# Optimization experiments

Measured on AMD Instinct MI355X. Metric: run time of the kernel, lower is better.

The kernel has to match this reference:

```python
import jax, jax.numpy as jnp
import numpy as np

_CLAMP = 1e6  # clamp bound for real/imag parts after each eml level
CPLX = jnp.complex64


def _eml_op(u, v):
    # eml(u, v) = exp(log(u) * log(v)) in complex arithmetic
    return jnp.exp(jnp.log(u) * jnp.log(v))


def _sanitize(z):
    r = jnp.clip(jnp.nan_to_num(z.real, nan=0.0, posinf=_CLAMP, neginf=-_CLAMP), -_CLAMP, _CLAMP)
    i = jnp.clip(jnp.nan_to_num(z.imag, nan=0.0, posinf=_CLAMP, neginf=-_CLAMP), -_CLAMP, _CLAMP)
    return jax.lax.complex(r, i)


def setup_inputs() -> dict:
    key = jax.random.key(0)
    k1, k2, k3 = jax.random.split(key, 3)
    depth = 10
    n_leaves = 2 ** depth          # 1024
    n_internal = n_leaves - 1      # 1023
    init_scale = 0.1
    batch = 65536
    x = jax.random.normal(k1, (batch,), jnp.float32)
    leaf = jax.random.normal(k2, (n_leaves, 2), jnp.float32) * init_scale
    leaf = leaf.at[:, 0].add(1.0)  # leaf_init[:, 0] += 1.0
    gate = jax.random.normal(k3, (n_internal, 2, 3), jnp.float32) * init_scale
    gate = gate.at[..., 2].add(1.0)  # gate_init[..., 2] += 1.0
    return {"x": x, "leaf_logits": leaf, "gate_logits": gate}


def reference(x, leaf_logits, gate_logits):
    xc = x.astype(CPLX)                      # [B]
    a = leaf_logits[:, 0].astype(CPLX)       # [L]
    b = leaf_logits[:, 1].astype(CPLX)       # [L]
    level = a[None, :] + b[None, :] * xc[:, None]   # [B, L] leaf inputs: alpha + beta*x
    x_b = xc[:, None]                        # [B, 1]
    g_all = gate_logits.astype(CPLX)         # [L-1, 2, 3]
    node_idx = 0
    while level.shape[1] > 1:
        n_pairs = level.shape[1] // 2
        left = level[:, 0::2]                # [B, n_pairs]
        right = level[:, 1::2]
        g = g_all[node_idx:node_idx + n_pairs]
        left_in = g[:, 0, 0][None] + g[:, 0, 1][None] * x_b + g[:, 0, 2][None] * left
        right_in = g[:, 1, 0][None] + g[:, 1, 1][None] * x_b + g[:, 1, 2][None] * right
        level = _sanitize(_eml_op(left_in, right_in))
        node_idx += n_pairs
    return level[:, 0]                       # [B] complex64
```

## Files before the change

kernel.cpp:

```cpp
#include <hip/hip_runtime.h>
#include <math.h>

#define CLAMPV 1000000.0f
#define PI_F     3.14159274f
#define HALFPI_F 1.57079633f
#define LN2_F    0.69314718f
#define L2E_F    1.44269504f
#define C1_F     0.17328680f
#define C2_F     0.05515890f
#define C2R_F    0.11031780f

typedef float v2f __attribute__((ext_vector_type(2)));

__device__ __forceinline__ v2f vb(float s) { return (v2f){s, s}; }
__device__ __forceinline__ v2f vfma(v2f a, v2f b, v2f c) { return __builtin_elementwise_fma(a, b, c); }

__device__ __forceinline__ const float* gptr(const float* __restrict__ g, int node) {
    return g + 6 * __builtin_amdgcn_readfirstlane(node);
}

__device__ __forceinline__ unsigned sortkey(float x) {
    unsigned u = __float_as_uint(x);
    u ^= (unsigned)(((int)u) >> 31) | 0x80000000u;
    return u;
}

__device__ __forceinline__ unsigned rank_below(unsigned long long m) {
    return __builtin_amdgcn_mbcnt_hi((unsigned)(m >> 32),
           __builtin_amdgcn_mbcnt_lo((unsigned)m, 0u));
}

__device__ __forceinline__ v2f fnode(v2f l, v2f r, v2f x,
                                     const float* __restrict__ g, v2f& tmin) {
    float g0 = g[0], g1 = g[1], g2 = g[2], g3 = g[3], g4 = g[4], g5 = g[5];
    v2f u = vfma(vb(g2), l, vfma(vb(g1), x, vb(g0)));
    v2f v = vfma(vb(g5), r, vfma(vb(g4), x, vb(g3)));
    tmin = __builtin_elementwise_min(tmin, __builtin_elementwise_min(u, v));
    v2f L2u = (v2f){__builtin_amdgcn_logf(u.x), __builtin_amdgcn_logf(u.y)};
    v2f L2v = (v2f){__builtin_amdgcn_logf(v.x), __builtin_amdgcn_logf(v.y)};
    v2f e = (vb(LN2_F) * L2u) * L2v;
    v2f rr = (v2f){__builtin_amdgcn_exp2f(e.x), __builtin_amdgcn_exp2f(e.y)};
    return __builtin_elementwise_min(rr, vb(CLAMPV));
}

__global__ __launch_bounds__(1024, 8) void eml_fast_taint(
    const float* __restrict__ x_g, const float* __restrict__ leaf_g,
    const float* __restrict__ gate_g, float* __restrict__ out,
    unsigned* __restrict__ cnt, unsigned* __restrict__ list,
    int batch, int out_real_only)
{
    __shared__ float4 s_t[16][64];

    const int lane = threadIdx.x;
    const int s    = threadIdx.y;
    const int e0 = blockIdx.x * 128 + lane;
    const v2f x2 = (v2f){x_g[e0], x_g[e0 + 64]};

    v2f tmin = vb(1.0f);
    v2f cA, cB, root;

#pragma clang loop unroll(disable)
    for (int q = 0; q < 4; ++q) {
        const int jq = 64 * s + 16 * q;
        v2f r2[2], h1, c;
#pragma unroll
        for (int p = 0; p < 4; ++p) {
            const int j = jq + 4 * p;
            const float* L = leaf_g + 2 * __builtin_amdgcn_readfirstlane(j);
            v2f l0 = vfma(vb(L[1]), x2, vb(L[0]));
            v2f l1 = vfma(vb(L[3]), x2, vb(L[2]));
            v2f l2 = vfma(vb(L[5]), x2, vb(L[4]));
            v2f l3 = vfma(vb(L[7]), x2, vb(L[6]));

            v2f A  = fnode(l0, l1, x2, gptr(gate_g, j >> 1), tmin);
            v2f B  = fnode(l2, l3, x2, gptr(gate_g, (j >> 1) + 1), tmin);
            v2f r1 = fnode(A, B, x2, gptr(gate_g, 512 + (j >> 2)), tmin);
            if (p & 1) r2[p >> 1] = fnode(h1, r1, x2, gptr(gate_g, 768 + (j >> 3)), tmin);
            else       h1 = r1;
        }
        c = fnode(r2[0], r2[1], x2, gptr(gate_g, 896 + (jq >> 4)), tmin);
        if      (q == 0) cA = c;
        else if (q == 1) cB = fnode(cA, c, x2, gptr(gate_g, 960 + 2 * s), tmin);
        else if (q == 2) cA = c;
        else {
            v2f t = fnode(cA, c, x2, gptr(gate_g, 961 + 2 * s), tmin);
            root  = fnode(cB, t, x2, gptr(gate_g, 992 + s), tmin);
        }
    }

    s_t[s][lane] = make_float4(root.x, root.y, tmin.x, tmin.y);
    __syncthreads();
    if (s != 0) return;

#pragma clang loop unroll(disable)
    for (int L = 6; L <= 9; ++L) {
        const int cntL = 1 << (9 - L);
        const int base = 1024 - (1 << (10 - L));
#pragma clang loop unroll(disable)
        for (int j = 0; j < cntL; ++j) {
            float4 a = s_t[2 * j][lane], b = s_t[2 * j + 1][lane];
            v2f tm = __builtin_elementwise_min((v2f){a.z, a.w}, (v2f){b.z, b.w});
            v2f r  = fnode((v2f){a.x, a.y}, (v2f){b.x, b.y}, x2,
                           gptr(gate_g, base + j), tm);
            s_t[j][lane] = make_float4(r.x, r.y, tm.x, tm.y);
        }
    }

    float4 fin = s_t[0][lane];
    const bool t0 = !(fin.z > 0.0f);
    const bool t1 = !(fin.w > 0.0f);

    if (!t0) {
        if (out_real_only) out[e0] = fin.x;
        else reinterpret_cast<float2*>(out)[e0] = make_float2(fin.x, 0.0f);
    }
    if (!t1) {
        if (out_real_only) out[e0 + 64] = fin.y;
        else reinterpret_cast<float2*>(out)[e0 + 64] = make_float2(fin.y, 0.0f);
    }

    unsigned long long m0 = __ballot(t0), m1 = __ballot(t1);
    int n0 = __popcll(m0), n1 = __popcll(m1);
    unsigned base = 0;
    if (lane == 0 && (n0 + n1)) base = atomicAdd(cnt, (unsigned)(n0 + n1));
    base = __shfl(base, 0);
    if (t0) list[base + rank_below(m0)] = (unsigned)e0;
    if (t1) list[base + n0 + rank_below(m1)] = (unsigned)(e0 + 64);
}

__global__ __launch_bounds__(1024) void eml_sort(
    const float* __restrict__ x_g, const unsigned* __restrict__ cnt,
    const unsigned* __restrict__ list, unsigned* __restrict__ list2)
{
    __shared__ unsigned hist[4096];
    __shared__ unsigned part[1024];
    const unsigned n = cnt[0];
    const int t = threadIdx.x;

    for (int i = t; i < 4096; i += 1024) hist[i] = 0u;
    __syncthreads();
    for (unsigned i = t; i < n; i += 1024)
        atomicAdd(&hist[sortkey(x_g[list[i]]) >> 20], 1u);
    __syncthreads();

    unsigned h0 = hist[4*t], h1 = hist[4*t+1], h2 = hist[4*t+2], h3 = hist[4*t+3];
    unsigned sum = h0 + h1 + h2 + h3;
    part[t] = sum;
    __syncthreads();
    for (int d = 1; d < 1024; d <<= 1) {
        unsigned v = (t >= d) ? part[t - d] : 0u;
        __syncthreads();
        part[t] += v;
        __syncthreads();
    }
    unsigned excl = part[t] - sum;
    hist[4*t]   = excl;
    hist[4*t+1] = excl + h0;
    hist[4*t+2] = excl + h0 + h1;
    hist[4*t+3] = excl + h0 + h1 + h2;
    __syncthreads();

    for (unsigned i = t; i < n; i += 1024) {
        unsigned id = list[i];
        unsigned pos = atomicAdd(&hist[sortkey(x_g[id]) >> 20], 1u);
        list2[pos] = id;
    }
}


__device__ __forceinline__ v2f sanitv(v2f v) {
    v2f c;
    c.x = __builtin_amdgcn_fmed3f(v.x, -CLAMPV, CLAMPV);
    c.y = __builtin_amdgcn_fmed3f(v.y, -CLAMPV, CLAMPV);
    c.x = (v.x != v.x) ? 0.0f : c.x;
    c.y = (v.y != v.y) ? 0.0f : c.y;
    return c;
}

__device__ __forceinline__ v2f fatan2v(v2f y, v2f x) {
    v2f ax = __builtin_elementwise_abs(x);
    v2f ay = __builtin_elementwise_abs(y);
    v2f mx = __builtin_elementwise_max(ax, ay);
    v2f mn = __builtin_elementwise_min(ax, ay);
    v2f r  = (v2f){__builtin_amdgcn_rcpf(mx.x), __builtin_amdgcn_rcpf(mx.y)};
    v2f t  = mn * r;
    v2f z  = t * t;
    v2f p  = vfma(z, vfma(z, vfma(z, vfma(z,
             vb(0.02083510f), vb(-0.08513300f)), vb(0.18014100f)), vb(-0.33029950f)),
             vb(0.99986600f));
    p = p * t;
    p.x = (ay.x > ax.x) ? (HALFPI_F - p.x) : p.x;
    p.y = (ay.y > ax.y) ? (HALFPI_F - p.y) : p.y;
    p.x = (x.x < 0.0f) ? (PI_F - p.x) : p.x;
    p.y = (x.y < 0.0f) ? (PI_F - p.y) : p.y;
    p.x = copysignf(p.x, y.x);
    p.y = copysignf(p.y, y.y);
    return p;
}

__device__ __forceinline__ void exp_tailv(v2f e, v2f f0, v2f& ore, v2f& oim) {
    v2f r = (v2f){__builtin_amdgcn_exp2f(e.x), __builtin_amdgcn_exp2f(e.y)};
    v2f f = (v2f){__builtin_amdgcn_fractf(f0.x), __builtin_amdgcn_fractf(f0.y)};
    v2f sn = (v2f){__builtin_amdgcn_sinf(f.x), __builtin_amdgcn_sinf(f.y)};
    v2f cs = (v2f){__builtin_amdgcn_cosf(f.x), __builtin_amdgcn_cosf(f.y)};
    ore = sanitv(r * cs);
    oim = sanitv(r * sn);
}

__device__ __forceinline__ void fast_rp(v2f ure, v2f vre, v2f& ore, v2f& oim) {
    v2f L2u = (v2f){__builtin_amdgcn_logf(ure.x), __builtin_amdgcn_logf(ure.y)};
    v2f L2v = (v2f){__builtin_amdgcn_logf(vre.x), __builtin_amdgcn_logf(vre.y)};
    v2f e = (vb(LN2_F) * L2u) * L2v;
    v2f r = (v2f){__builtin_amdgcn_exp2f(e.x), __builtin_amdgcn_exp2f(e.y)};
    v2f c = __builtin_elementwise_min(r, vb(CLAMPV));
    c.x = (r.x != r.x) ? 0.0f : c.x;
    c.y = (r.y != r.y) ? 0.0f : c.y;
    ore = c;
    oim = vb(0.0f);
}

__device__ __forceinline__ void node_any(
    v2f lre, v2f lim, v2f rre, v2f rim,
    v2f x, const float* __restrict__ g,
    v2f& ore, v2f& oim)
{
    float g0 = g[0], g1 = g[1], g2 = g[2], g3 = g[3], g4 = g[4], g5 = g[5];
    v2f ure = vfma(vb(g2), lre, vfma(vb(g1), x, vb(g0)));
    v2f vre = vfma(vb(g5), rre, vfma(vb(g4), x, vb(g3)));
    v2f mn = __builtin_elementwise_min(ure, vre);

    unsigned long long bad =
        __ballot(lim.x != 0.0f) | __ballot(lim.y != 0.0f) |
        __ballot(rim.x != 0.0f) | __ballot(rim.y != 0.0f) |
        __ballot(mn.x <= 0.0f)  | __ballot(mn.y <= 0.0f);

    if (bad == 0ULL) {
        fast_rp(ure, vre, ore, oim);
    } else {
        v2f uim = vfma(vb(g2), lim, vb(0.0f));
        v2f vim = vfma(vb(g5), rim, vb(0.0f));

        v2f nu = vfma(ure, ure, uim * uim);
        v2f nv = vfma(vre, vre, vim * vim);
        v2f L2u = (v2f){__builtin_amdgcn_logf(nu.x), __builtin_amdgcn_logf(nu.y)};
        v2f L2v = (v2f){__builtin_amdgcn_logf(nv.x), __builtin_amdgcn_logf(nv.y)};
        v2f Au = fatan2v(uim, ure);
        v2f Av = fatan2v(vim, vre);

        v2f t2 = vb(L2E_F) * (Au * Av);
        v2f e  = vfma(vb(C1_F) * L2u, L2v, -t2);
        v2f s2 = vfma(L2u, Av, Au * L2v);
        v2f f0 = vb(C2_F) * s2;
        exp_tailv(e, f0, ore, oim);
    }
}

__device__ __forceinline__ void node_r0(
    v2f l, v2f r, v2f x, const float* __restrict__ g,
    v2f& ore, v2f& oim)
{
    float g0 = g[0], g1 = g[1], g2 = g[2], g3 = g[3], g4 = g[4], g5 = g[5];
    v2f u = vfma(vb(g2), l, vfma(vb(g1), x, vb(g0)));
    v2f v = vfma(vb(g5), r, vfma(vb(g4), x, vb(g3)));
    v2f mn = __builtin_elementwise_min(u, v);

    unsigned long long bad = __ballot(mn.x <= 0.0f) | __ballot(mn.y <= 0.0f);

    if (bad == 0ULL) {
        fast_rp(u, v, ore, oim);
    } else {
        v2f au = __builtin_elementwise_abs(u);
        v2f av = __builtin_elementwise_abs(v);
        v2f L2u = (v2f){__builtin_amdgcn_logf(au.x), __builtin_amdgcn_logf(au.y)};
        v2f L2v = (v2f){__builtin_amdgcn_logf(av.x), __builtin_amdgcn_logf(av.y)};
        v2f Au, Av;
        Au.x = (u.x < 0.0f) ? PI_F : 0.0f;
        Au.y = (u.y < 0.0f) ? PI_F : 0.0f;
        Av.x = (v.x < 0.0f) ? PI_F : 0.0f;
        Av.y = (v.y < 0.0f) ? PI_F : 0.0f;

        v2f t2 = vb(L2E_F) * (Au * Av);
        v2f e  = vfma(vb(LN2_F) * L2u, L2v, -t2);
        v2f s2 = vfma(L2u, Av, Au * L2v);
        v2f f0 = vb(C2R_F) * s2;
        exp_tailv(e, f0, ore, oim);
    }
}

__global__ __launch_bounds__(1024, 8) void eml_slow(
    const float* __restrict__ x_g, const float* __restrict__ leaf_g,
    const float* __restrict__ gate_g, const unsigned* __restrict__ cnt,
    const unsigned* __restrict__ list, float* __restrict__ out,
    int batch, int out_real_only)
{
    __shared__ float4 s_t[16][64];

    const unsigned count = cnt[0];
    const unsigned r0 = blockIdx.x * 128u;
    if (r0 >= count) return;

    const int lane = threadIdx.x;
    const int s    = threadIdx.y;
    const unsigned ra = min(r0 + (unsigned)lane, count - 1u);
    const unsigned rb = min(r0 + (unsigned)lane + 64u, count - 1u);
    const unsigned ia = list[ra], ib = list[rb];
    const v2f x2 = (v2f){x_g[ia], x_g[ib]};

    v2f cAre, cAim, cBre, cBim, rootre, rootim;

#pragma clang loop unroll(disable)
    for (int q = 0; q < 4; ++q) {
        const int jq = 64 * s + 16 * q;
        v2f r2re[2], r2im[2];
        v2f h1re = vb(0.0f), h1im = vb(0.0f);
        v2f cre, cim;

#pragma unroll
        for (int p = 0; p < 4; ++p) {
            const int j = jq + 4 * p;
            const float* L = leaf_g + 2 * __builtin_amdgcn_readfirstlane(j);
            v2f l0 = vfma(vb(L[1]), x2, vb(L[0]));
            v2f l1 = vfma(vb(L[3]), x2, vb(L[2]));
            v2f l2 = vfma(vb(L[5]), x2, vb(L[4]));
            v2f l3 = vfma(vb(L[7]), x2, vb(L[6]));

            v2f Are, Aim, Bre, Bim;
            node_r0(l0, l1, x2, gptr(gate_g, j >> 1), Are, Aim);
            node_r0(l2, l3, x2, gptr(gate_g, (j >> 1) + 1), Bre, Bim);

            v2f r1re, r1im;
            node_any(Are, Aim, Bre, Bim, x2, gptr(gate_g, 512 + (j >> 2)), r1re, r1im);

            if (p & 1) {
                node_any(h1re, h1im, r1re, r1im, x2,
                         gptr(gate_g, 768 + (j >> 3)), r2re[p >> 1], r2im[p >> 1]);
            } else {
                h1re = r1re; h1im = r1im;
            }
        }
        node_any(r2re[0], r2im[0], r2re[1], r2im[1], x2,
                 gptr(gate_g, 896 + (jq >> 4)), cre, cim);

        if (q == 0) {
            cAre = cre; cAim = cim;
        } else if (q == 1) {
            node_any(cAre, cAim, cre, cim, x2, gptr(gate_g, 960 + 2 * s), cBre, cBim);
        } else if (q == 2) {
            cAre = cre; cAim = cim;
        } else {
            v2f tre, tim;
            node_any(cAre, cAim, cre, cim, x2, gptr(gate_g, 961 + 2 * s), tre, tim);
            node_any(cBre, cBim, tre, tim, x2, gptr(gate_g, 992 + s), rootre, rootim);
        }
    }

    s_t[s][lane] = make_float4(rootre.x, rootre.y, rootim.x, rootim.y);
    __syncthreads();
    if (s != 0) return;

#pragma clang loop unroll(disable)
    for (int L = 6; L <= 9; ++L) {
        const int cntL = 1 << (9 - L);
        const int base = 1024 - (1 << (10 - L));
#pragma clang loop unroll(disable)
        for (int j = 0; j < cntL; ++j) {
            float4 a = s_t[2 * j][lane], b = s_t[2 * j + 1][lane];
            v2f rre, rim;
            node_any((v2f){a.x, a.y}, (v2f){a.z, a.w},
                     (v2f){b.x, b.y}, (v2f){b.z, b.w},
                     x2, gptr(gate_g, base + j), rre, rim);
            s_t[j][lane] = make_float4(rre.x, rre.y, rim.x, rim.y);
        }
    }

    float4 fin = s_t[0][lane];
    if (out_real_only) {
        out[ia] = fin.x;
        out[ib] = fin.y;
    } else {
        reinterpret_cast<float2*>(out)[ia] = make_float2(fin.x, fin.z);
        reinterpret_cast<float2*>(out)[ib] = make_float2(fin.y, fin.w);
    }
}

extern "C" void kernel_launch(void* const* d_in, const int* in_sizes, int n_in,
                              void* d_out, int out_size, void* d_ws, size_t ws_size,
                              hipStream_t stream) {
    const float* x    = (const float*)d_in[0];
    const float* leaf = (const float*)d_in[1];
    const float* gate = (const float*)d_in[2];
    float* out = (float*)d_out;
    const int batch = in_sizes[0];

    const int out_real_only = (out_size == batch) ? 1 : 0;

    unsigned* cnt   = (unsigned*)d_ws;
    unsigned* list  = (unsigned*)d_ws + 64;
    unsigned* list2 = list + batch;
    const size_t need_sort = (64 + 2 * (size_t)batch) * sizeof(unsigned);
    const bool do_sort = (ws_size >= need_sort);

    hipMemsetAsync(cnt, 0, sizeof(unsigned), stream);

    dim3 block(64, 16);
    dim3 grid(batch / 128);
    hipLaunchKernelGGL(eml_fast_taint, grid, block, 0, stream,
                       x, leaf, gate, out, cnt, list, batch, out_real_only);
    if (do_sort) {
        hipLaunchKernelGGL(eml_sort, dim3(1), dim3(1024), 0, stream,
                           x, cnt, list, list2);
    }
    hipLaunchKernelGGL(eml_slow, grid, block, 0, stream,
                       x, leaf, gate, cnt,
                       do_sort ? list2 : list, out, batch, out_real_only);
}
```

Measured before the change: 136.1 us.

## Process four elements per thread in fast pass and split sort into parallel kernels

The fast taint kernel now handles four batch elements per thread (two v2f pairs), which halves the grid and reuses each gate and leaf scalar load across more work. Occupancy bounds drop to compensate for the higher register use. The single-block sort is replaced by three steps: histogram atomics in global memory issued from the fast kernel, a one-block scan kernel, and a grid-wide scatter kernel. This removes the serial single-workgroup histogram and scatter passes, at the cost of global atomics, an extra launch and a larger memset.

Measured after the change: 154.1 us. 1.13x slower.

```diff
diff --git a/kernel.cpp b/kernel.cpp
--- a/kernel.cpp
+++ b/kernel.cpp
@@ -43,52 +43,68 @@
     return __builtin_elementwise_min(rr, vb(CLAMPV));
 }
 
-__global__ __launch_bounds__(1024, 8) void eml_fast_taint(
+struct P { v2f a, b; };
+__device__ __forceinline__ P fnode2(P l, P r, v2f xa, v2f xb,
+                                    const float* __restrict__ g,
+                                    v2f& tma, v2f& tmb) {
+    P o;
+    o.a = fnode(l.a, r.a, xa, g, tma);
+    o.b = fnode(l.b, r.b, xb, g, tmb);
+    return o;
+}
+__device__ __forceinline__ P leaf2(float aa, float bb, v2f xa, v2f xb) {
+    P o; o.a = vfma(vb(bb), xa, vb(aa)); o.b = vfma(vb(bb), xb, vb(aa)); return o;
+}
+
+__global__ __launch_bounds__(1024, 4) void eml_fast_taint(
     const float* __restrict__ x_g, const float* __restrict__ leaf_g,
     const float* __restrict__ gate_g, float* __restrict__ out,
-    unsigned* __restrict__ cnt, unsigned* __restrict__ list,
-    int batch, int out_real_only)
-{
-    __shared__ float4 s_t[16][64];
+    unsigned* __restrict__ cnt, unsigned* __restrict__ hist,
+    unsigned* __restrict__ list, int batch, int out_real_only)
+{
+    __shared__ float4 sA[16][64];
+    __shared__ float4 sB[16][64];
 
     const int lane = threadIdx.x;
     const int s    = threadIdx.y;
-    const int e0 = blockIdx.x * 128 + lane;
-    const v2f x2 = (v2f){x_g[e0], x_g[e0 + 64]};
-
-    v2f tmin = vb(1.0f);
-    v2f cA, cB, root;
+    const int e0 = blockIdx.x * 256 + lane;
+    const v2f xa = (v2f){x_g[e0],       x_g[e0 + 64]};
+    const v2f xb = (v2f){x_g[e0 + 128], x_g[e0 + 192]};
+
+    v2f tma = vb(1.0f), tmb = vb(1.0f);
+    P cA, cB, root;
 
 #pragma clang loop unroll(disable)
     for (int q = 0; q < 4; ++q) {
         const int jq = 64 * s + 16 * q;
-        v2f r2[2], h1, c;
+        P r2[2], h1, c;
 #pragma unroll
         for (int p = 0; p < 4; ++p) {
             const int j = jq + 4 * p;
             const float* L = leaf_g + 2 * __builtin_amdgcn_readfirstlane(j);
-            v2f l0 = vfma(vb(L[1]), x2, vb(L[0]));
-            v2f l1 = vfma(vb(L[3]), x2, vb(L[2]));
-            v2f l2 = vfma(vb(L[5]), x2, vb(L[4]));
-            v2f l3 = vfma(vb(L[7]), x2, vb(L[6]));
-
-            v2f A  = fnode(l0, l1, x2, gptr(gate_g, j >> 1), tmin);
-            v2f B  = fnode(l2, l3, x2, gptr(gate_g, (j >> 1) + 1), tmin);
-            v2f r1 = fnode(A, B, x2, gptr(gate_g, 512 + (j >> 2)), tmin);
-            if (p & 1) r2[p >> 1] = fnode(h1, r1, x2, gptr(gate_g, 768 + (j >> 3)), tmin);
+            P l0 = leaf2(L[0], L[1], xa, xb);
+            P l1 = leaf2(L[2], L[3], xa, xb);
+            P l2 = leaf2(L[4], L[5], xa, xb);
+            P l3 = leaf2(L[6], L[7], xa, xb);
+
+            P A  = fnode2(l0, l1, xa, xb, gptr(gate_g, j >> 1), tma, tmb);
+            P B  = fnode2(l2, l3, xa, xb, gptr(gate_g, (j >> 1) + 1), tma, tmb);
+            P r1 = fnode2(A, B, xa, xb, gptr(gate_g, 512 + (j >> 2)), tma, tmb);
+            if (p & 1) r2[p >> 1] = fnode2(h1, r1, xa, xb, gptr(gate_g, 768 + (j >> 3)), tma, tmb);
             else       h1 = r1;
         }
-        c = fnode(r2[0], r2[1], x2, gptr(gate_g, 896 + (jq >> 4)), tmin);
+        c = fnode2(r2[0], r2[1], xa, xb, gptr(gate_g, 896 + (jq >> 4)), tma, tmb);
         if      (q == 0) cA = c;
-        else if (q == 1) cB = fnode(cA, c, x2, gptr(gate_g, 960 + 2 * s), tmin);
+        else if (q == 1) cB = fnode2(cA, c, xa, xb, gptr(gate_g, 960 + 2 * s), tma, tmb);
         else if (q == 2) cA = c;
         else {
-            v2f t = fnode(cA, c, x2, gptr(gate_g, 961 + 2 * s), tmin);
-            root  = fnode(cB, t, x2, gptr(gate_g, 992 + s), tmin);
-        }
-    }
-
-    s_t[s][lane] = make_float4(root.x, root.y, tmin.x, tmin.y);
+            P t  = fnode2(cA, c, xa, xb, gptr(gate_g, 961 + 2 * s), tma, tmb);
+            root = fnode2(cB, t, xa, xb, gptr(gate_g, 992 + s), tma, tmb);
+        }
+    }
+
+    sA[s][lane] = make_float4(root.a.x, root.a.y, tma.x, tma.y);
+    sB[s][lane] = make_float4(root.b.x, root.b.y, tmb.x, tmb.y);
     __syncthreads();
     if (s != 0) return;
 
@@ -98,51 +114,60 @@
         const int base = 1024 - (1 << (10 - L));
 #pragma clang loop unroll(disable)
         for (int j = 0; j < cntL; ++j) {
-            float4 a = s_t[2 * j][lane], b = s_t[2 * j + 1][lane];
-            v2f tm = __builtin_elementwise_min((v2f){a.z, a.w}, (v2f){b.z, b.w});
-            v2f r  = fnode((v2f){a.x, a.y}, (v2f){b.x, b.y}, x2,
-                           gptr(gate_g, base + j), tm);
-            s_t[j][lane] = make_float4(r.x, r.y, tm.x, tm.y);
-        }
-    }
-
-    float4 fin = s_t[0][lane];
-    const bool t0 = !(fin.z > 0.0f);
-    const bool t1 = !(fin.w > 0.0f);
-
-    if (!t0) {
-        if (out_real_only) out[e0] = fin.x;
-        else reinterpret_cast<float2*>(out)[e0] = make_float2(fin.x, 0.0f);
-    }
-    if (!t1) {
-        if (out_real_only) out[e0 + 64] = fin.y;
-        else reinterpret_cast<float2*>(out)[e0 + 64] = make_float2(fin.y, 0.0f);
+            const float* g = gptr(gate_g, base + j);
+            float4 a0 = sA[2 * j][lane], a1 = sA[2 * j + 1][lane];
+            v2f ta = __builtin_elementwise_min((v2f){a0.z, a0.w}, (v2f){a1.z, a1.w});
+            v2f ra = fnode((v2f){a0.x, a0.y}, (v2f){a1.x, a1.y}, xa, g, ta);
+            sA[j][lane] = make_float4(ra.x, ra.y, ta.x, ta.y);
+
+            float4 b0 = sB[2 * j][lane], b1 = sB[2 * j + 1][lane];
+            v2f tb = __builtin_elementwise_min((v2f){b0.z, b0.w}, (v2f){b1.z, b1.w});
+            v2f rb = fnode((v2f){b0.x, b0.y}, (v2f){b1.x, b1.y}, xb, g, tb);
+            sB[j][lane] = make_float4(rb.x, rb.y, tb.x, tb.y);
+        }
+    }
+
+    float4 fa = sA[0][lane], fb = sB[0][lane];
+    const bool t0 = !(fa.z > 0.0f);
+    const bool t1 = !(fa.w > 0.0f);
+    const bool t2 = !(fb.z > 0.0f);
+    const bool t3 = !(fb.w > 0.0f);
+
+    if (out_real_only) {
+        if (!t0) out[e0]       = fa.x;
+        if (!t1) out[e0 + 64]  = fa.y;
+        if (!t2) out[e0 + 128] = fb.x;
+        if (!t3) out[e0 + 192] = fb.y;
+    } else {
+        float2* o2 = reinterpret_cast<float2*>(out);
+        if (!t0) o2[e0]       = make_float2(fa.x, 0.0f);
+        if (!t1) o2[e0 + 64]  = make_float2(fa.y, 0.0f);
+        if (!t2) o2[e0 + 128] = make_float2(fb.x, 0.0f);
+        if (!t3) o2[e0 + 192] = make_float2(fb.y, 0.0f);
     }
 
     unsigned long long m0 = __ballot(t0), m1 = __ballot(t1);
-    int n0 = __popcll(m0), n1 = __popcll(m1);
+    unsigned long long m2 = __ballot(t2), m3 = __ballot(t3);
+    int n0 = __popcll(m0), n1 = __popcll(m1), n2 = __popcll(m2), n3 = __popcll(m3);
     unsigned base = 0;
-    if (lane == 0 && (n0 + n1)) base = atomicAdd(cnt, (unsigned)(n0 + n1));
+    int tot = n0 + n1 + n2 + n3;
+    if (lane == 0 && tot) base = atomicAdd(cnt, (unsigned)tot);
     base = __shfl(base, 0);
-    if (t0) list[base + rank_below(m0)] = (unsigned)e0;
-    if (t1) list[base + n0 + rank_below(m1)] = (unsigned)(e0 + 64);
-}
-
-__global__ __launch_bounds__(1024) void eml_sort(
-    const float* __restrict__ x_g, const unsigned* __restrict__ cnt,
-    const unsigned* __restrict__ list, unsigned* __restrict__ list2)
-{
-    __shared__ unsigned hist[4096];
+    if (t0) { list[base + rank_below(m0)] = (unsigned)e0;
+              atomicAdd(&hist[sortkey(xa.x) >> 20], 1u); }
+    if (t1) { list[base + n0 + rank_below(m1)] = (unsigned)(e0 + 64);
+              atomicAdd(&hist[sortkey(xa.y) >> 20], 1u); }
+    if (t2) { list[base + n0 + n1 + rank_below(m2)] = (unsigned)(e0 + 128);
+              atomicAdd(&hist[sortkey(xb.x) >> 20], 1u); }
+    if (t3) { list[base + n0 + n1 + n2 + rank_below(m3)] = (unsigned)(e0 + 192);
+              atomicAdd(&hist[sortkey(xb.y) >> 20], 1u); }
+}
+
+__global__ __launch_bounds__(1024) void eml_scan(
+    const unsigned* __restrict__ hist, unsigned* __restrict__ offs)
+{
     __shared__ unsigned part[1024];
-    const unsigned n = cnt[0];
     const int t = threadIdx.x;
-
-    for (int i = t; i < 4096; i += 1024) hist[i] = 0u;
-    __syncthreads();
-    for (unsigned i = t; i < n; i += 1024)
-        atomicAdd(&hist[sortkey(x_g[list[i]]) >> 20], 1u);
-    __syncthreads();
-
     unsigned h0 = hist[4*t], h1 = hist[4*t+1], h2 = hist[4*t+2], h3 = hist[4*t+3];
     unsigned sum = h0 + h1 + h2 + h3;
     part[t] = sum;
@@ -154,15 +179,22 @@
         __syncthreads();
     }
     unsigned excl = part[t] - sum;
-    hist[4*t]   = excl;
-    hist[4*t+1] = excl + h0;
-    hist[4*t+2] = excl + h0 + h1;
-    hist[4*t+3] = excl + h0 + h1 + h2;
-    __syncthreads();
-
-    for (unsigned i = t; i < n; i += 1024) {
+    offs[4*t]   = excl;
+    offs[4*t+1] = excl + h0;
+    offs[4*t+2] = excl + h0 + h1;
+    offs[4*t+3] = excl + h0 + h1 + h2;
+}
+
+__global__ __launch_bounds__(256) void eml_scatter(
+    const float* __restrict__ x_g, const unsigned* __restrict__ cnt,
+    const unsigned* __restrict__ list, unsigned* __restrict__ offs,
+    unsigned* __restrict__ list2)
+{
+    const unsigned n = cnt[0];
+    const unsigned i = blockIdx.x * 256u + threadIdx.x;
+    if (i < n) {
         unsigned id = list[i];
-        unsigned pos = atomicAdd(&hist[sortkey(x_g[id]) >> 20], 1u);
+        unsigned pos = atomicAdd(&offs[sortkey(x_g[id]) >> 20], 1u);
         list2[pos] = id;
     }
 }
@@ -395,22 +427,24 @@
     const int out_real_only = (out_size == batch) ? 1 : 0;
 
     unsigned* cnt   = (unsigned*)d_ws;
-    unsigned* list  = (unsigned*)d_ws + 64;
+    unsigned* hist  = cnt + 64;
+    unsigned* offs  = hist + 4096;
+    unsigned* list  = offs + 4096;
     unsigned* list2 = list + batch;
-    const size_t need_sort = (64 + 2 * (size_t)batch) * sizeof(unsigned);
-    const bool do_sort = (ws_size >= need_sort);
-
-    hipMemsetAsync(cnt, 0, sizeof(unsigned), stream);
+    const size_t need_full = (64 + 4096 + 4096 + 2 * (size_t)batch) * sizeof(unsigned);
+    const bool do_sort = (ws_size >= need_full);
+
+    hipMemsetAsync(cnt, 0, (64 + 4096) * sizeof(unsigned), stream);
 
     dim3 block(64, 16);
-    dim3 grid(batch / 128);
-    hipLaunchKernelGGL(eml_fast_taint, grid, block, 0, stream,
-                       x, leaf, gate, out, cnt, list, batch, out_real_only);
+    hipLaunchKernelGGL(eml_fast_taint, dim3(batch / 256), block, 0, stream,
+                       x, leaf, gate, out, cnt, hist, list, batch, out_real_only);
     if (do_sort) {
-        hipLaunchKernelGGL(eml_sort, dim3(1), dim3(1024), 0, stream,
-                           x, cnt, list, list2);
-    }
-    hipLaunchKernelGGL(eml_slow, grid, block, 0, stream,
+        hipLaunchKernelGGL(eml_scan, dim3(1), dim3(1024), 0, stream, hist, offs);
+        hipLaunchKernelGGL(eml_scatter, dim3((batch + 255) / 256), dim3(256), 0, stream,
+                           x, cnt, list, offs, list2);
+    }
+    hipLaunchKernelGGL(eml_slow, dim3(batch / 128), block, 0, stream,
                        x, leaf, gate, cnt,
                        do_sort ? list2 : list, out, batch, out_real_only);
 }
```
